# Performance work log

Hardware: AMD Instinct MI355X
Metric: run time of the kernel (lower is better)

Reference implementation:

```python
import jax, jax.numpy as jnp
import numpy as np

N_NODES = 100000
N_EDGES = 1600000
DIM_IN, DIM_H, DIM_OUT = 64, 64, 16


def setup_inputs() -> dict:
    key = jax.random.key(0)
    ks = jax.random.split(key, 7)
    s = lambda d: 1.0 / np.sqrt(d)
    return {
        "x": jax.random.normal(ks[0], (N_NODES, DIM_IN), dtype=jnp.float32),
        "edge_index": jax.random.randint(ks[1], (2, N_EDGES), 0, N_NODES, dtype=jnp.int32),
        "W1l": jax.random.normal(ks[2], (DIM_IN, DIM_H), dtype=jnp.float32) * s(DIM_IN),
        "W1r": jax.random.normal(ks[3], (DIM_IN, DIM_H), dtype=jnp.float32) * s(DIM_IN),
        "b1": jnp.zeros((DIM_H,), dtype=jnp.float32),
        "W2l": jax.random.normal(ks[4], (DIM_H, DIM_OUT), dtype=jnp.float32) * s(DIM_H),
        "W2r": jax.random.normal(ks[5], (DIM_H, DIM_OUT), dtype=jnp.float32) * s(DIM_H),
        "b2": jnp.zeros((DIM_OUT,), dtype=jnp.float32),
    }


def _sage_conv(h, edge_index, Wl, Wr, b):
    # PyG SAGEConv (mean aggr): out = mean_{j in N(i)} h_j @ Wl + h_i @ Wr + b
    src, dst = edge_index[0], edge_index[1]
    n = h.shape[0]
    agg = jax.ops.segment_sum(h[src], dst, num_segments=n)          # [N, d]
    deg = jax.ops.segment_sum(jnp.ones_like(dst, dtype=h.dtype), dst, num_segments=n)
    mean = agg / jnp.maximum(deg, 1.0)[:, None]
    return mean @ Wl + h @ Wr + b


def reference(x, edge_index, W1l, W1r, b1, W2l, W2r, b2):
    h = jax.nn.relu(_sage_conv(x, edge_index, W1l, W1r, b1))
    # dropout(p=0.5) is identity in eval mode (training=False)
    h = _sage_conv(h, edge_index, W2l, W2r, b2)
    return jax.nn.log_softmax(h, axis=1)
```

## Files before the change

kernel.cpp:

```cpp
#include <hip/hip_runtime.h>
#include <cstdint>
#include <cstddef>


typedef float f32x4 __attribute__((ext_vector_type(4)));
typedef float f32x2 __attribute__((ext_vector_type(2)));
typedef short short8 __attribute__((ext_vector_type(8)));
typedef __bf16 bf16x8 __attribute__((ext_vector_type(8)));

#define BK 256
#define NBMAX 512
#define CAP 5120
#define TILE 8192

__device__ __forceinline__ unsigned f2bf(float f) {
    unsigned u = __float_as_uint(f);
    u += 0x7FFFu + ((u >> 16) & 1u);
    return u >> 16;
}

__device__ __forceinline__ f32x4 mfma16(short8 a, short8 b, f32x4 c) {
    return __builtin_amdgcn_mfma_f32_16x16x32_bf16(
        __builtin_bit_cast(bf16x8, a), __builtin_bit_cast(bf16x8, b), c, 0, 0, 0);
}

#define ACC2(r, alo, ahi)                     \
    alo += __uint_as_float((r) << 16);        \
    ahi += __uint_as_float(r);

#define ACCF8(w, i)                                                   \
    {                                                                 \
        f32x2 f0 = __builtin_amdgcn_cvt_pk_f32_fp8((w), false);       \
        f32x2 f1 = __builtin_amdgcn_cvt_pk_f32_fp8((w), true);        \
        acc[(i)] += f0.x; acc[(i) + 1] += f0.y;                       \
        acc[(i) + 2] += f1.x; acc[(i) + 3] += f1.y;                   \
    }

__global__ __launch_bounds__(512) void partprep_k(
    const int* __restrict__ ei, int* __restrict__ bcnt,
    unsigned* __restrict__ part, int E, int pblocks,
    const float* __restrict__ x, unsigned short* __restrict__ xb,
    unsigned char* __restrict__ xq, int n,
    const float* __restrict__ W1l, const float* __restrict__ W1r,
    const float* __restrict__ W2l, const float* __restrict__ W2r,
    unsigned short* __restrict__ bimg, int xblocks) {
    __shared__ int scn[NBMAX], sbase[NBMAX], lofs[NBMAX], cur[NBMAX];
    __shared__ unsigned stageW[TILE];
    __shared__ unsigned short stageB[TILE];
    int t = threadIdx.x;
    int bid = blockIdx.x;

    if (bid >= pblocks) {
        int cb = bid - pblocks;
        if (cb < xblocks) {
            int i = (cb * 512 + t) * 8;
            if (i >= n) return;
            const float4* xp = (const float4*)(x + i);
            float4 a = xp[0], b = xp[1];
            uint4 o;
            o.x = f2bf(a.x) | (f2bf(a.y) << 16);
            o.y = f2bf(a.z) | (f2bf(a.w) << 16);
            o.z = f2bf(b.x) | (f2bf(b.y) << 16);
            o.w = f2bf(b.z) | (f2bf(b.w) << 16);
            *(uint4*)(xb + i) = o;
            int w0 = __builtin_amdgcn_cvt_pk_fp8_f32(a.x, a.y, 0, false);
            w0 = __builtin_amdgcn_cvt_pk_fp8_f32(a.z, a.w, w0, true);
            int w1 = __builtin_amdgcn_cvt_pk_fp8_f32(b.x, b.y, 0, false);
            w1 = __builtin_amdgcn_cvt_pk_fp8_f32(b.z, b.w, w1, true);
            *(uint2*)(xq + i) = make_uint2((unsigned)w0, (unsigned)w1);
            return;
        }
        int e = (cb - xblocks) * 512 + t;
        if (e >= 20 * 64) return;
        int f = e >> 6, L = e & 63;
        int qd = L >> 4, m = L & 15;
        unsigned o[8];
        if (f < 16) {
            int kb = f >> 2, nb = f & 3;
            int n2 = nb * 16 + m;
#pragma unroll
            for (int j = 0; j < 8; ++j) {
                int k = kb * 32 + qd * 8 + j;
                float v = (k < 64) ? W1l[k * 64 + n2] : W1r[(k - 64) * 64 + n2];
                o[j] = f2bf(v);
            }
        } else {
            int g = f - 16;
            int kb = g >> 1, nb = g & 1;
#pragma unroll
            for (int j = 0; j < 8; ++j) {
                int k = kb * 32 + qd * 8 + j;
                float v = nb ? W2r[k * 16 + m] : W2l[k * 16 + m];
                o[j] = f2bf(v);
            }
        }
        uint4 pk;
        pk.x = o[0] | (o[1] << 16);
        pk.y = o[2] | (o[3] << 16);
        pk.z = o[4] | (o[5] << 16);
        pk.w = o[6] | (o[7] << 16);
        ((uint4*)bimg)[e] = pk;
        return;
    }

    int base = bid * TILE;
    cur[t] = 0;
    __syncthreads();
    int4 s4[4], d4[4];
#pragma unroll
    for (int i = 0; i < 4; ++i) {
        int e0 = base + (t + i * 512) * 4;
        if (e0 < E) {
            s4[i] = ((const int4*)ei)[e0 >> 2];
            d4[i] = ((const int4*)(ei + E))[e0 >> 2];
        } else {
            d4[i] = make_int4(-1, -1, -1, -1);
            s4[i] = make_int4(0, 0, 0, 0);
        }
    }
    int rk[16];
#pragma unroll
    for (int i = 0; i < 4; ++i) {
        int d[4] = {d4[i].x, d4[i].y, d4[i].z, d4[i].w};
#pragma unroll
        for (int u = 0; u < 4; ++u)
            rk[i * 4 + u] = (d[u] >= 0) ? atomicAdd(&cur[d[u] >> 8], 1) : 0;
    }
    __syncthreads();
    int own = cur[t];
    scn[t] = own;
    __syncthreads();
    for (int off = 1; off < NBMAX; off <<= 1) {
        int v = (t >= off) ? scn[t - off] : 0;
        __syncthreads();
        scn[t] += v;
        __syncthreads();
    }
    lofs[t] = scn[t] - own;
    if (own > 0) sbase[t] = atomicAdd(&bcnt[t], own);
    __syncthreads();
#pragma unroll
    for (int i = 0; i < 4; ++i) {
        int s[4] = {s4[i].x, s4[i].y, s4[i].z, s4[i].w};
        int d[4] = {d4[i].x, d4[i].y, d4[i].z, d4[i].w};
#pragma unroll
        for (int u = 0; u < 4; ++u) {
            if (d[u] < 0) continue;
            int b = d[u] >> 8;
            int pos = lofs[b] + rk[i * 4 + u];
            stageW[pos] = ((unsigned)(d[u] & (BK - 1)) << 17) | (unsigned)s[u];
            stageB[pos] = (unsigned short)b;
        }
    }
    __syncthreads();
    int tot = scn[NBMAX - 1];
    for (int q = t; q < tot; q += 512) {
        int b = stageB[q];
        part[b * CAP + sbase[b] + (q - lofs[b])] = stageW[q];
    }
}

__global__ __launch_bounds__(256) void csr_k(const unsigned* __restrict__ part,
                                             const int* __restrict__ bcnt,
                                             int* __restrict__ csr,
                                             int2* __restrict__ rowse, int N) {
    __shared__ int h[BK];
    __shared__ int s[BK];
    int b = blockIdx.x, t = threadIdx.x;
    int cnt = bcnt[b];
    int base = b * CAP;
    h[t] = 0;
    __syncthreads();
    for (int q = t; q < cnt; q += 256)
        atomicAdd(&h[(part[base + q] >> 17) & (BK - 1)], 1);
    __syncthreads();
    int own = h[t];
    s[t] = own;
    __syncthreads();
    for (int off = 1; off < BK; off <<= 1) {
        int v = (t >= off) ? s[t - off] : 0;
        __syncthreads();
        s[t] += v;
        __syncthreads();
    }
    int excl = s[t] - own;
    int node = b * BK + t;
    if (node < N) rowse[node] = make_int2(base + excl, base + excl + own);
    __syncthreads();
    h[t] = excl;
    __syncthreads();
    for (int q = t; q < cnt; q += 256) {
        unsigned w = part[base + q];
        int pos = atomicAdd(&h[(w >> 17) & (BK - 1)], 1);
        csr[base + pos] = (int)(w & 0x1FFFFu);
    }
}

__global__ __launch_bounds__(256, 6) void l1x(
    const unsigned short* __restrict__ xb, const unsigned char* __restrict__ xq,
    const int2* __restrict__ rowse, const int* __restrict__ csr,
    const unsigned short* __restrict__ bimg,
    const float* __restrict__ b1, const float* __restrict__ b2,
    unsigned short* __restrict__ p, float* __restrict__ q, int N) {
    __shared__ unsigned short mh[4][16][72];
    int t = threadIdx.x;
    int wave = t >> 6, lane = t & 63;
    int nodebase = blockIdx.x * 64 + wave * 16;
    int grp = lane >> 2, sub = lane & 3;
    int node = nodebase + grp;
    int2 be = (node < N) ? rowse[node] : make_int2(0, 0);

    float acc[16];
#pragma unroll
    for (int i = 0; i < 16; ++i) acc[i] = 0.f;
    int k = be.x, kend = be.y;
    for (; k + 3 < kend; k += 4) {
        int s0 = csr[k], s1 = csr[k + 1], s2 = csr[k + 2], s3 = csr[k + 3];
        uint4 a = ((const uint4*)(xq + ((size_t)s0 << 6)))[sub];
        uint4 b = ((const uint4*)(xq + ((size_t)s1 << 6)))[sub];
        uint4 c = ((const uint4*)(xq + ((size_t)s2 << 6)))[sub];
        uint4 d = ((const uint4*)(xq + ((size_t)s3 << 6)))[sub];
        ACCF8(a.x, 0); ACCF8(a.y, 4); ACCF8(a.z, 8); ACCF8(a.w, 12);
        ACCF8(b.x, 0); ACCF8(b.y, 4); ACCF8(b.z, 8); ACCF8(b.w, 12);
        ACCF8(c.x, 0); ACCF8(c.y, 4); ACCF8(c.z, 8); ACCF8(c.w, 12);
        ACCF8(d.x, 0); ACCF8(d.y, 4); ACCF8(d.z, 8); ACCF8(d.w, 12);
    }
    if (k + 1 < kend) {
        int s0 = csr[k], s1 = csr[k + 1];
        uint4 a = ((const uint4*)(xq + ((size_t)s0 << 6)))[sub];
        uint4 b = ((const uint4*)(xq + ((size_t)s1 << 6)))[sub];
        ACCF8(a.x, 0); ACCF8(a.y, 4); ACCF8(a.z, 8); ACCF8(a.w, 12);
        ACCF8(b.x, 0); ACCF8(b.y, 4); ACCF8(b.z, 8); ACCF8(b.w, 12);
        k += 2;
    }
    if (k < kend) {
        int s0 = csr[k];
        uint4 a = ((const uint4*)(xq + ((size_t)s0 << 6)))[sub];
        ACCF8(a.x, 0); ACCF8(a.y, 4); ACCF8(a.z, 8); ACCF8(a.w, 12);
    }
    {
        float rd = 1.0f / fmaxf((float)(be.y - be.x), 1.0f);
        uint4 o0, o1;
        o0.x = f2bf(acc[0] * rd) | (f2bf(acc[1] * rd) << 16);
        o0.y = f2bf(acc[2] * rd) | (f2bf(acc[3] * rd) << 16);
        o0.z = f2bf(acc[4] * rd) | (f2bf(acc[5] * rd) << 16);
        o0.w = f2bf(acc[6] * rd) | (f2bf(acc[7] * rd) << 16);
        o1.x = f2bf(acc[8] * rd) | (f2bf(acc[9] * rd) << 16);
        o1.y = f2bf(acc[10] * rd) | (f2bf(acc[11] * rd) << 16);
        o1.z = f2bf(acc[12] * rd) | (f2bf(acc[13] * rd) << 16);
        o1.w = f2bf(acc[14] * rd) | (f2bf(acc[15] * rd) << 16);
        *(uint4*)&mh[wave][grp][sub * 16] = o0;
        *(uint4*)&mh[wave][grp][sub * 16 + 8] = o1;
    }

    int qd = lane >> 4, m = lane & 15;
    int mynode = nodebase + m;
    const short8* bfr = (const short8*)bimg;
    short8 afr0 = *(const short8*)&mh[wave][m][qd * 8];
    short8 afr1 = *(const short8*)&mh[wave][m][32 + qd * 8];
    short8 afr2 = {0, 0, 0, 0, 0, 0, 0, 0};
    short8 afr3 = {0, 0, 0, 0, 0, 0, 0, 0};
    if (mynode < N) {
        afr2 = *(const short8*)(xb + ((size_t)mynode << 6) + qd * 8);
        afr3 = *(const short8*)(xb + ((size_t)mynode << 6) + 32 + qd * 8);
    }

#pragma unroll
    for (int nb = 0; nb < 4; ++nb) {
        f32x4 c = {0.f, 0.f, 0.f, 0.f};
        c = mfma16(afr0, bfr[nb * 64 + lane], c);
        c = mfma16(afr1, bfr[(4 + nb) * 64 + lane], c);
        c = mfma16(afr2, bfr[(8 + nb) * 64 + lane], c);
        c = mfma16(afr3, bfr[(12 + nb) * 64 + lane], c);
        int col = nb * 16 + m;
        float bb = b1[col];
#pragma unroll
        for (int r = 0; r < 4; ++r) {
            float hv = fmaxf(c[r] + bb, 0.0f);
            mh[wave][qd * 4 + r][col] = (unsigned short)f2bf(hv);
        }
    }

    short8 ha0 = *(const short8*)&mh[wave][m][qd * 8];
    short8 ha1 = *(const short8*)&mh[wave][m][32 + qd * 8];
    f32x4 pc = {0.f, 0.f, 0.f, 0.f}, qc = {0.f, 0.f, 0.f, 0.f};
    pc = mfma16(ha0, bfr[16 * 64 + lane], pc);
    pc = mfma16(ha1, bfr[18 * 64 + lane], pc);
    qc = mfma16(ha0, bfr[17 * 64 + lane], qc);
    qc = mfma16(ha1, bfr[19 * 64 + lane], qc);
    float b2v = b2[m];
#pragma unroll
    for (int r = 0; r < 4; ++r) {
        int nd = nodebase + qd * 4 + r;
        if (nd < N) {
            p[(size_t)nd * 16 + m] = (unsigned short)f2bf(pc[r]);
            q[(size_t)nd * 16 + m] = qc[r] + b2v;
        }
    }
}

__global__ __launch_bounds__(256) void finalk(const unsigned short* __restrict__ p,
                                              const int2* __restrict__ rowse,
                                              const int* __restrict__ csr,
                                              float* q, int N) {
    int t = threadIdx.x;
    int wave = t >> 6, lane = t & 63;
    int grp = lane >> 2, sub = lane & 3;
    int node = blockIdx.x * 64 + wave * 16 + grp;
    if (node >= N) return;
    int2 be = rowse[node];
    float4 qv = ((const float4*)(q + ((size_t)node << 4)))[sub];
    float a0 = 0.f, a1 = 0.f, a2 = 0.f, a3 = 0.f;
    int k = be.x, kend = be.y;
    for (; k + 3 < kend; k += 4) {
        int s0 = csr[k], s1 = csr[k + 1], s2 = csr[k + 2], s3 = csr[k + 3];
        uint2 rA = *(const uint2*)(p + ((size_t)s0 << 4) + (sub << 2));
        uint2 rB = *(const uint2*)(p + ((size_t)s1 << 4) + (sub << 2));
        uint2 rC = *(const uint2*)(p + ((size_t)s2 << 4) + (sub << 2));
        uint2 rD = *(const uint2*)(p + ((size_t)s3 << 4) + (sub << 2));
        ACC2(rA.x, a0, a1);  ACC2(rA.y, a2, a3);
        ACC2(rB.x, a0, a1);  ACC2(rB.y, a2, a3);
        ACC2(rC.x, a0, a1);  ACC2(rC.y, a2, a3);
        ACC2(rD.x, a0, a1);  ACC2(rD.y, a2, a3);
    }
    if (k + 1 < kend) {
        int s0 = csr[k], s1 = csr[k + 1];
        uint2 rA = *(const uint2*)(p + ((size_t)s0 << 4) + (sub << 2));
        uint2 rB = *(const uint2*)(p + ((size_t)s1 << 4) + (sub << 2));
        ACC2(rA.x, a0, a1);  ACC2(rA.y, a2, a3);
        ACC2(rB.x, a0, a1);  ACC2(rB.y, a2, a3);
        k += 2;
    }
    if (k < kend) {
        int s0 = csr[k];
        uint2 rA = *(const uint2*)(p + ((size_t)s0 << 4) + (sub << 2));
        ACC2(rA.x, a0, a1);  ACC2(rA.y, a2, a3);
    }
    float rd = 1.0f / fmaxf((float)(be.y - be.x), 1.0f);
    float4 v = {a0 * rd + qv.x, a1 * rd + qv.y, a2 * rd + qv.z, a3 * rd + qv.w};
    float mm = fmaxf(fmaxf(v.x, v.y), fmaxf(v.z, v.w));
    mm = fmaxf(mm, __shfl_xor(mm, 1));
    mm = fmaxf(mm, __shfl_xor(mm, 2));
    float s = __expf(v.x - mm) + __expf(v.y - mm) + __expf(v.z - mm) + __expf(v.w - mm);
    s += __shfl_xor(s, 1);
    s += __shfl_xor(s, 2);
    float ls = __logf(s);
    float4 o = {v.x - mm - ls, v.y - mm - ls, v.z - mm - ls, v.w - mm - ls};
    ((float4*)(q + ((size_t)node << 4)))[sub] = o;
}

extern "C" void kernel_launch(void* const* d_in, const int* in_sizes, int n_in,
                              void* d_out, int out_size, void* d_ws, size_t ws_size,
                              hipStream_t stream) {
    const float* x   = (const float*)d_in[0];
    const int* ei    = (const int*)d_in[1];
    const float* W1l = (const float*)d_in[2];
    const float* W1r = (const float*)d_in[3];
    const float* b1  = (const float*)d_in[4];
    const float* W2l = (const float*)d_in[5];
    const float* W2r = (const float*)d_in[6];
    const float* b2  = (const float*)d_in[7];
    const int N = in_sizes[0] / 64;
    const int E = in_sizes[1] / 2;
    const int nbk = (N + BK - 1) / BK;

    int*  bcnt  = (int*)d_ws;
    int2* rowse = (int2*)(bcnt + NBMAX);
    int*  csr   = (int*)(rowse + N);
    unsigned short* bimg = (unsigned short*)(csr + (size_t)nbk * CAP);
    unsigned short* p    = bimg + 20 * 64 * 8;
    unsigned* part = (unsigned*)(p + (size_t)N * 16);
    unsigned short* xb = (unsigned short*)(part + (size_t)nbk * CAP);
    unsigned char* xq = (unsigned char*)(xb + (size_t)N * 64);
    float* q = (float*)d_out;

    hipMemsetAsync(bcnt, 0, NBMAX * sizeof(int), stream);

    const int pblocks = (E + TILE - 1) / TILE;
    const int xblocks = (N * 64 + 4095) / 4096;
    partprep_k<<<pblocks + xblocks + 3, 512, 0, stream>>>(
        ei, bcnt, part, E, pblocks, x, xb, xq, N * 64, W1l, W1r, W2l, W2r,
        bimg, xblocks);
    csr_k<<<nbk, 256, 0, stream>>>(part, bcnt, csr, rowse, N);
    l1x<<<(N + 63) / 64, 256, 0, stream>>>(xb, xq, rowse, csr, bimg, b1, b2,
                                           p, q, N);
    finalk<<<(N + 63) / 64, 256, 0, stream>>>(p, rowse, csr, q, N);
}
```

Measured before the change: 179.6 us.

## Split layer-1 fp8 gather into two feature-half passes for cache locality

Stores the fp8 node features as two separate 32-byte-per-node halves and gathers the first half in a new kernel that writes bf16 means into the reused partition buffer. The layer-1 kernel then gathers only the second half and reads the precomputed first-half mean for its MFMA. The point is to halve the working set of each random gather so it fits better in L2/MALL, at the cost of an extra launch, a second CSR walk and an extra write/read of the mean buffer. The occupancy hint on l1x is also changed from 6 to 4.

```diff
diff --git a/kernel.cpp b/kernel.cpp
--- a/kernel.cpp
+++ b/kernel.cpp
@@ -40,7 +40,7 @@
     const int* __restrict__ ei, int* __restrict__ bcnt,
     unsigned* __restrict__ part, int E, int pblocks,
     const float* __restrict__ x, unsigned short* __restrict__ xb,
-    unsigned char* __restrict__ xq, int n,
+    unsigned char* __restrict__ xqA, unsigned char* __restrict__ xqB, int n,
     const float* __restrict__ W1l, const float* __restrict__ W1r,
     const float* __restrict__ W2l, const float* __restrict__ W2r,
     unsigned short* __restrict__ bimg, int xblocks) {
@@ -67,7 +67,10 @@
             w0 = __builtin_amdgcn_cvt_pk_fp8_f32(a.z, a.w, w0, true);
             int w1 = __builtin_amdgcn_cvt_pk_fp8_f32(b.x, b.y, 0, false);
             w1 = __builtin_amdgcn_cvt_pk_fp8_f32(b.z, b.w, w1, true);
-            *(uint2*)(xq + i) = make_uint2((unsigned)w0, (unsigned)w1);
+            int node = i >> 6, feat = i & 63;
+            unsigned char* dst = (feat < 32) ? (xqA + (size_t)node * 32 + feat)
+                                             : (xqB + (size_t)node * 32 + (feat - 32));
+            *(uint2*)dst = make_uint2((unsigned)w0, (unsigned)w1);
             return;
         }
         int e = (cb - xblocks) * 512 + t;
@@ -196,8 +199,55 @@
     }
 }
 
-__global__ __launch_bounds__(256, 6) void l1x(
-    const unsigned short* __restrict__ xb, const unsigned char* __restrict__ xq,
+__global__ __launch_bounds__(256) void gathA(
+    const unsigned char* __restrict__ xqA, const int2* __restrict__ rowse,
+    const int* __restrict__ csr, unsigned short* __restrict__ meanA, int N) {
+    int t = threadIdx.x;
+    int wave = t >> 6, lane = t & 63;
+    int grp = lane >> 2, sub = lane & 3;
+    int node = blockIdx.x * 64 + wave * 16 + grp;
+    if (node >= N) return;
+    int2 be = rowse[node];
+    float acc[8];
+#pragma unroll
+    for (int i = 0; i < 8; ++i) acc[i] = 0.f;
+    int k = be.x, kend = be.y;
+    for (; k + 3 < kend; k += 4) {
+        int s0 = csr[k], s1 = csr[k + 1], s2 = csr[k + 2], s3 = csr[k + 3];
+        uint2 a = *(const uint2*)(xqA + ((size_t)s0 << 5) + (sub << 3));
+        uint2 b = *(const uint2*)(xqA + ((size_t)s1 << 5) + (sub << 3));
+        uint2 c = *(const uint2*)(xqA + ((size_t)s2 << 5) + (sub << 3));
+        uint2 d = *(const uint2*)(xqA + ((size_t)s3 << 5) + (sub << 3));
+        ACCF8(a.x, 0); ACCF8(a.y, 4);
+        ACCF8(b.x, 0); ACCF8(b.y, 4);
+        ACCF8(c.x, 0); ACCF8(c.y, 4);
+        ACCF8(d.x, 0); ACCF8(d.y, 4);
+    }
+    if (k + 1 < kend) {
+        int s0 = csr[k], s1 = csr[k + 1];
+        uint2 a = *(const uint2*)(xqA + ((size_t)s0 << 5) + (sub << 3));
+        uint2 b = *(const uint2*)(xqA + ((size_t)s1 << 5) + (sub << 3));
+        ACCF8(a.x, 0); ACCF8(a.y, 4);
+        ACCF8(b.x, 0); ACCF8(b.y, 4);
+        k += 2;
+    }
+    if (k < kend) {
+        int s0 = csr[k];
+        uint2 a = *(const uint2*)(xqA + ((size_t)s0 << 5) + (sub << 3));
+        ACCF8(a.x, 0); ACCF8(a.y, 4);
+    }
+    float rd = 1.0f / fmaxf((float)(be.y - be.x), 1.0f);
+    uint4 o;
+    o.x = f2bf(acc[0] * rd) | (f2bf(acc[1] * rd) << 16);
+    o.y = f2bf(acc[2] * rd) | (f2bf(acc[3] * rd) << 16);
+    o.z = f2bf(acc[4] * rd) | (f2bf(acc[5] * rd) << 16);
+    o.w = f2bf(acc[6] * rd) | (f2bf(acc[7] * rd) << 16);
+    *(uint4*)(meanA + ((size_t)node << 5) + (sub << 3)) = o;
+}
+
+__global__ __launch_bounds__(256, 4) void l1x(
+    const unsigned short* __restrict__ xb, const unsigned char* __restrict__ xqB,
+    const unsigned short* __restrict__ meanA,
     const int2* __restrict__ rowse, const int* __restrict__ csr,
     const unsigned short* __restrict__ bimg,
     const float* __restrict__ b1, const float* __restrict__ b2,
@@ -210,57 +260,53 @@
     int node = nodebase + grp;
     int2 be = (node < N) ? rowse[node] : make_int2(0, 0);
 
-    float acc[16];
-#pragma unroll
-    for (int i = 0; i < 16; ++i) acc[i] = 0.f;
+    float acc[8];
+#pragma unroll
+    for (int i = 0; i < 8; ++i) acc[i] = 0.f;
     int k = be.x, kend = be.y;
     for (; k + 3 < kend; k += 4) {
         int s0 = csr[k], s1 = csr[k + 1], s2 = csr[k + 2], s3 = csr[k + 3];
-        uint4 a = ((const uint4*)(xq + ((size_t)s0 << 6)))[sub];
-        uint4 b = ((const uint4*)(xq + ((size_t)s1 << 6)))[sub];
-        uint4 c = ((const uint4*)(xq + ((size_t)s2 << 6)))[sub];
-        uint4 d = ((const uint4*)(xq + ((size_t)s3 << 6)))[sub];
-        ACCF8(a.x, 0); ACCF8(a.y, 4); ACCF8(a.z, 8); ACCF8(a.w, 12);
-        ACCF8(b.x, 0); ACCF8(b.y, 4); ACCF8(b.z, 8); ACCF8(b.w, 12);
-        ACCF8(c.x, 0); ACCF8(c.y, 4); ACCF8(c.z, 8); ACCF8(c.w, 12);
-        ACCF8(d.x, 0); ACCF8(d.y, 4); ACCF8(d.z, 8); ACCF8(d.w, 12);
+        uint2 a = *(const uint2*)(xqB + ((size_t)s0 << 5) + (sub << 3));
+        uint2 b = *(const uint2*)(xqB + ((size_t)s1 << 5) + (sub << 3));
+        uint2 c = *(const uint2*)(xqB + ((size_t)s2 << 5) + (sub << 3));
+        uint2 d = *(const uint2*)(xqB + ((size_t)s3 << 5) + (sub << 3));
+        ACCF8(a.x, 0); ACCF8(a.y, 4);
+        ACCF8(b.x, 0); ACCF8(b.y, 4);
+        ACCF8(c.x, 0); ACCF8(c.y, 4);
+        ACCF8(d.x, 0); ACCF8(d.y, 4);
     }
     if (k + 1 < kend) {
         int s0 = csr[k], s1 = csr[k + 1];
-        uint4 a = ((const uint4*)(xq + ((size_t)s0 << 6)))[sub];
-        uint4 b = ((const uint4*)(xq + ((size_t)s1 << 6)))[sub];
-        ACCF8(a.x, 0); ACCF8(a.y, 4); ACCF8(a.z, 8); ACCF8(a.w, 12);
-        ACCF8(b.x, 0); ACCF8(b.y, 4); ACCF8(b.z, 8); ACCF8(b.w, 12);
+        uint2 a = *(const uint2*)(xqB + ((size_t)s0 << 5) + (sub << 3));
+        uint2 b = *(const uint2*)(xqB + ((size_t)s1 << 5) + (sub << 3));
+        ACCF8(a.x, 0); ACCF8(a.y, 4);
+        ACCF8(b.x, 0); ACCF8(b.y, 4);
         k += 2;
     }
     if (k < kend) {
         int s0 = csr[k];
-        uint4 a = ((const uint4*)(xq + ((size_t)s0 << 6)))[sub];
-        ACCF8(a.x, 0); ACCF8(a.y, 4); ACCF8(a.z, 8); ACCF8(a.w, 12);
+        uint2 a = *(const uint2*)(xqB + ((size_t)s0 << 5) + (sub << 3));
+        ACCF8(a.x, 0); ACCF8(a.y, 4);
     }
     {
         float rd = 1.0f / fmaxf((float)(be.y - be.x), 1.0f);
-        uint4 o0, o1;
-        o0.x = f2bf(acc[0] * rd) | (f2bf(acc[1] * rd) << 16);
-        o0.y = f2bf(acc[2] * rd) | (f2bf(acc[3] * rd) << 16);
-        o0.z = f2bf(acc[4] * rd) | (f2bf(acc[5] * rd) << 16);
-        o0.w = f2bf(acc[6] * rd) | (f2bf(acc[7] * rd) << 16);
-        o1.x = f2bf(acc[8] * rd) | (f2bf(acc[9] * rd) << 16);
-        o1.y = f2bf(acc[10] * rd) | (f2bf(acc[11] * rd) << 16);
-        o1.z = f2bf(acc[12] * rd) | (f2bf(acc[13] * rd) << 16);
-        o1.w = f2bf(acc[14] * rd) | (f2bf(acc[15] * rd) << 16);
-        *(uint4*)&mh[wave][grp][sub * 16] = o0;
-        *(uint4*)&mh[wave][grp][sub * 16 + 8] = o1;
+        uint4 o;
+        o.x = f2bf(acc[0] * rd) | (f2bf(acc[1] * rd) << 16);
+        o.y = f2bf(acc[2] * rd) | (f2bf(acc[3] * rd) << 16);
+        o.z = f2bf(acc[4] * rd) | (f2bf(acc[5] * rd) << 16);
+        o.w = f2bf(acc[6] * rd) | (f2bf(acc[7] * rd) << 16);
+        *(uint4*)&mh[wave][grp][sub * 8] = o;
     }
 
     int qd = lane >> 4, m = lane & 15;
     int mynode = nodebase + m;
     const short8* bfr = (const short8*)bimg;
-    short8 afr0 = *(const short8*)&mh[wave][m][qd * 8];
-    short8 afr1 = *(const short8*)&mh[wave][m][32 + qd * 8];
+    short8 afr0 = {0, 0, 0, 0, 0, 0, 0, 0};
+    short8 afr1 = *(const short8*)&mh[wave][m][qd * 8];
     short8 afr2 = {0, 0, 0, 0, 0, 0, 0, 0};
     short8 afr3 = {0, 0, 0, 0, 0, 0, 0, 0};
     if (mynode < N) {
+        afr0 = *(const short8*)(meanA + ((size_t)mynode << 5) + qd * 8);
         afr2 = *(const short8*)(xb + ((size_t)mynode << 6) + qd * 8);
         afr3 = *(const short8*)(xb + ((size_t)mynode << 6) + 32 + qd * 8);
     }
@@ -370,8 +416,10 @@
     unsigned short* bimg = (unsigned short*)(csr + (size_t)nbk * CAP);
     unsigned short* p    = bimg + 20 * 64 * 8;
     unsigned* part = (unsigned*)(p + (size_t)N * 16);
+    unsigned short* meanA = (unsigned short*)part;
     unsigned short* xb = (unsigned short*)(part + (size_t)nbk * CAP);
-    unsigned char* xq = (unsigned char*)(xb + (size_t)N * 64);
+    unsigned char* xqA = (unsigned char*)(xb + (size_t)N * 64);
+    unsigned char* xqB = xqA + (size_t)N * 32;
     float* q = (float*)d_out;
 
     hipMemsetAsync(bcnt, 0, NBMAX * sizeof(int), stream);
@@ -379,10 +427,11 @@
     const int pblocks = (E + TILE - 1) / TILE;
     const int xblocks = (N * 64 + 4095) / 4096;
     partprep_k<<<pblocks + xblocks + 3, 512, 0, stream>>>(
-        ei, bcnt, part, E, pblocks, x, xb, xq, N * 64, W1l, W1r, W2l, W2r,
-        bimg, xblocks);
+        ei, bcnt, part, E, pblocks, x, xb, xqA, xqB, N * 64, W1l, W1r, W2l,
+        W2r, bimg, xblocks);
     csr_k<<<nbk, 256, 0, stream>>>(part, bcnt, csr, rowse, N);
-    l1x<<<(N + 63) / 64, 256, 0, stream>>>(xb, xq, rowse, csr, bimg, b1, b2,
-                                           p, q, N);
+    gathA<<<(N + 63) / 64, 256, 0, stream>>>(xqA, rowse, csr, meanA, N);
+    l1x<<<(N + 63) / 64, 256, 0, stream>>>(xb, xqB, meanA, rowse, csr, bimg,
+                                           b1, b2, p, q, N);
     finalk<<<(N + 63) / 64, 256, 0, stream>>>(p, rowse, csr, q, N);
 }
```

Measured after the change: 170.5 us. -5.1%, faster.
